# Performance work log

Hardware: AMD Instinct MI355X
Metric: run time of the kernel (lower is better)

Reference implementation:

```python
import jax, jax.numpy as jnp
import numpy as np

DIM = 192; HEADS = 6; WIN = 8; HIDDEN = int(DIM * 2.66); EPS = 1e-5

def dct_matrix(n):
    # DCT-II orthonormal matrix, matches get_dctMatrix(n, n)
    i = np.arange(n)[:, None]; j = np.arange(n)[None, :]
    M = np.cos(np.pi * i * (2 * j + 1) / (2 * n)) * np.sqrt(2.0 / n)
    M[0, :] = np.sqrt(1.0 / n)
    return jnp.asarray(M, dtype=jnp.float32)

def layernorm_c(x, w, b):
    # WithBias LayerNorm over channel dim of BCHW (restormer to_3d/to_4d style)
    mu = x.mean(axis=1, keepdims=True)
    var = ((x - mu) ** 2).mean(axis=1, keepdims=True)
    return (x - mu) / jnp.sqrt(var + EPS) * w[None, :, None, None] + b[None, :, None, None]

def conv1x1(x, w, b=None):
    y = jnp.einsum('oc,bchw->bohw', w, x)
    return y if b is None else y + b[None, :, None, None]

def dwconv3x3(x, w):
    return jax.lax.conv_general_dilated(x, w, (1, 1), ((1, 1), (1, 1)),
        dimension_numbers=('NCHW', 'OIHW', 'NCHW'), feature_group_count=x.shape[1])

def l2norm(x):
    n = jnp.sqrt(jnp.sum(x * x, axis=-1, keepdims=True))
    return x / jnp.maximum(n, 1e-12)

def window_channel_attn(qkv, temperature):
    # 'b (z head c) (h1 h) (w1 w) -> z (b h1 w1) head c (h w)'
    b, _, H, W = qkv.shape
    cph = DIM // HEADS
    h1, w1 = H // WIN, W // WIN
    t = qkv.reshape(b, 3, HEADS, cph, h1, WIN, w1, WIN)
    t = t.transpose(1, 0, 4, 6, 2, 3, 5, 7).reshape(3, b * h1 * w1, HEADS, cph, WIN * WIN)
    q, k, v = t[0], t[1], t[2]
    q = l2norm(q); k = l2norm(k)
    attn = jnp.einsum('nhce,nhde->nhcd', q, k) * temperature[None]  # channel x channel per window
    attn = jax.nn.softmax(attn, axis=-1)
    out = jnp.einsum('nhcd,nhde->nhce', attn, v)
    out = out.reshape(b, h1, w1, HEADS, cph, WIN, WIN)
    out = out.transpose(0, 3, 4, 1, 5, 2, 6).reshape(b, DIM, H, W)
    return out

def forward(x, norm1_w, norm1_b, w_qkv, w_dw, temperature, w_proj, b_proj,
            norm2_w, norm2_b, w_in, w_dwf, w_out):
    B, C, H, W = x.shape
    Mh = dct_matrix(H); Mw = dct_matrix(W)
    # attention branch in DCT domain
    y = layernorm_c(x, norm1_w, norm1_b)
    y = jnp.einsum('ph,bchw->bcpw', Mh, y)      # dct2dx: Mh @ y @ Mw.T
    y = jnp.einsum('bcpw,qw->bcpq', y, Mw)
    qkv = dwconv3x3(conv1x1(y, w_qkv), w_dw)
    a = window_channel_attn(qkv, temperature)
    a = conv1x1(a, w_proj, b_proj)
    a = jnp.einsum('bcpq,qw->bcpw', a, Mw)      # idct2dx: Mh.T @ a @ Mw
    a = jnp.einsum('bcpw,ph->bchw', a, Mh)
    x1 = x + a
    # gated-dconv FFN branch
    z = layernorm_c(x1, norm2_w, norm2_b)
    f = dwconv3x3(conv1x1(z, w_in), w_dwf)
    f1, f2 = jnp.split(f, 2, axis=1)
    f = jax.nn.gelu(f1, approximate=False) * f2
    f = conv1x1(f, w_out)
    return x1 + f

def setup_inputs() -> dict:
    key = jax.random.key(0)
    ks = jax.random.split(key, 8)
    B, C, H, W = 2, DIM, 192, 192
    s = 0.02
    return {
        'x': jax.random.normal(ks[0], (B, C, H, W), jnp.float32),
        'norm1_w': jnp.ones((C,), jnp.float32),
        'norm1_b': jnp.zeros((C,), jnp.float32),
        'w_qkv': jax.random.normal(ks[1], (3 * C, C), jnp.float32) * s,
        'w_dw': jax.random.normal(ks[2], (3 * C, 1, 3, 3), jnp.float32) * s,
        'temperature': jnp.ones((HEADS, 1, 1), jnp.float32) / np.float32(np.sqrt(C)),
        'w_proj': jax.random.normal(ks[3], (C, C), jnp.float32) * s,
        'b_proj': jnp.zeros((C,), jnp.float32),
        'norm2_w': jnp.ones((C,), jnp.float32),
        'norm2_b': jnp.zeros((C,), jnp.float32),
        'w_in': jax.random.normal(ks[4], (2 * HIDDEN, C), jnp.float32) * s,
        'w_dwf': jax.random.normal(ks[5], (2 * HIDDEN, 1, 3, 3), jnp.float32) * s,
        'w_out': jax.random.normal(ks[6], (C, HIDDEN), jnp.float32) * s,
    }

def reference(x, norm1_w, norm1_b, w_qkv, w_dw, temperature, w_proj, b_proj,
              norm2_w, norm2_b, w_in, w_dwf, w_out):
    return forward(x, norm1_w, norm1_b, w_qkv, w_dw, temperature, w_proj, b_proj,
                   norm2_w, norm2_b, w_in, w_dwf, w_out)
```

## Files before the change

### kernel.cpp

```cpp
#include <hip/hip_runtime.h>
#include <hip/hip_bf16.h>

typedef __hip_bfloat16 bft;
typedef __attribute__((ext_vector_type(8))) short bf16x8;
typedef __attribute__((ext_vector_type(4))) float f32x4;

#define BLK 256
static constexpr int Cc = 192;
static constexpr int L  = 192;
static constexpr int S  = 36864;
static constexpr int Bn = 2;
static constexpr int HID = 510;
static constexpr int CH = 64;
static constexpr int FTR = (CH + 2) * L;
static constexpr int GTR = CH * L;
static constexpr double PI_D = 3.141592653589793238462643383279502884;

__device__ __forceinline__ float ldf(const float* p) { return *p; }
__device__ __forceinline__ float ldf(const bft* p)   { return __bfloat162float(*p); }
__device__ __forceinline__ void  stf(float* p, float v) { *p = v; }
__device__ __forceinline__ void  stf(bft* p, float v)   { *p = __float2bfloat16(v); }
__device__ __forceinline__ unsigned short f2bfu(float f) {
    bft h = __float2bfloat16(f);
    return *reinterpret_cast<const unsigned short*>(&h);
}
__device__ __forceinline__ unsigned short bfu(const bft* p) {
    return *reinterpret_cast<const unsigned short*>(p);
}
__device__ __forceinline__ float bu2f(unsigned short u) {
    unsigned int x = (unsigned int)u << 16;
    return __uint_as_float(x);
}
__device__ __forceinline__ bf16x8 ld8(const unsigned short* p) {
    union { unsigned int u[4]; bf16x8 v; } t;
    const unsigned int* q = reinterpret_cast<const unsigned int*>(p);
    t.u[0] = q[0]; t.u[1] = q[1]; t.u[2] = q[2]; t.u[3] = q[3];
    return t.v;
}

__global__ __launch_bounds__(BLK) void k_dct_init(bft* __restrict__ dctb,
                                                  bft* __restrict__ dctTb) {
    int idx = blockIdx.x * BLK + threadIdx.x;
    if (idx >= L * L) return;
    int p = idx / L, h = idx - p * L;
    double v = (p == 0) ? sqrt(1.0 / L)
                        : cos(PI_D * p * (2 * h + 1) / (2.0 * L)) * sqrt(2.0 / L);
    bft bv = __float2bfloat16((float)v);
    dctb[p * L + h] = bv;
    dctTb[h * L + p] = bv;
}

__global__ __launch_bounds__(BLK) void k_cvt(const float* __restrict__ src,
                                             bft* __restrict__ dst,
                                             int Mr, int Kr, int Kp) {
    int idx = blockIdx.x * BLK + threadIdx.x;
    int m = idx / Kp, k = idx - m * Kp;
    float v = (m < Mr && k < Kr) ? src[(size_t)m * Kr + k] : 0.f;
    dst[idx] = __float2bfloat16(v);
}

__global__ __launch_bounds__(BLK) void k_cvt_ffn(const float* __restrict__ src,
                                                 bft* __restrict__ dst) {
    int idx = blockIdx.x * BLK + threadIdx.x;
    int m = idx / Cc, k = idx - m * Cc;
    float v = 0.f;
    if (m < 510) v = src[(size_t)m * Cc + k];
    else if (m >= 512 && m < 1022) v = src[(size_t)(m - 2) * Cc + k];
    dst[idx] = __float2bfloat16(v);
}

template <typename TI>
__global__ __launch_bounds__(BLK) void k_ln8(const TI* __restrict__ x,
                                             const float* __restrict__ w,
                                             const float* __restrict__ b,
                                             bft* __restrict__ out,
                                             long zI, long zO) {
    int t = blockIdx.x * BLK + threadIdx.x;
    int s = t >> 3, u = t & 7;
    const TI* xp = x + (size_t)blockIdx.y * zI + s;
    bft* op = out + (size_t)blockIdx.y * zO;
    float vals[24];
    float sum = 0.f, sq = 0.f;
#pragma unroll
    for (int j = 0; j < 24; ++j) {
        vals[j] = ldf(xp + (size_t)(u * 24 + j) * S);
        sum += vals[j]; sq += vals[j] * vals[j];
    }
#pragma unroll
    for (int m = 1; m < 8; m <<= 1) {
        sum += __shfl_xor(sum, m);
        sq  += __shfl_xor(sq, m);
    }
    float mu = sum * (1.f / Cc);
    float var = sq * (1.f / Cc) - mu * mu;
    float r = rsqrtf(var + 1e-5f);
#pragma unroll
    for (int j = 0; j < 24; ++j) {
        int c = u * 24 + j;
        stf(op + (size_t)c * S + s, (vals[j] - mu) * r * w[c] + b[c]);
    }
}

template <typename TI>
__global__ __launch_bounds__(BLK) void k_lnT8(const TI* __restrict__ x,
                                              const float* __restrict__ w,
                                              const float* __restrict__ b,
                                              bft* __restrict__ out,
                                              long zI, long zO) {
    int t = blockIdx.x * BLK + threadIdx.x;
    int s = t >> 3, u = t & 7;
    const TI* xp = x + (size_t)blockIdx.y * zI + s;
    float vals[24];
    float sum = 0.f, sq = 0.f;
#pragma unroll
    for (int j = 0; j < 24; ++j) {
        vals[j] = ldf(xp + (size_t)(u * 24 + j) * S);
        sum += vals[j]; sq += vals[j] * vals[j];
    }
#pragma unroll
    for (int m = 1; m < 8; m <<= 1) {
        sum += __shfl_xor(sum, m);
        sq  += __shfl_xor(sq, m);
    }
    float mu = sum * (1.f / Cc);
    float var = sq * (1.f / Cc) - mu * mu;
    float r = rsqrtf(var + 1e-5f);
    bft* op = out + (size_t)blockIdx.y * zO + (size_t)s * Cc + u * 24;
#pragma unroll
    for (int q = 0; q < 3; ++q) {
        unsigned short v8[8];
#pragma unroll
        for (int jj = 0; jj < 8; ++jj) {
            int c = u * 24 + q * 8 + jj;
            v8[jj] = f2bfu((vals[q * 8 + jj] - mu) * r * w[c] + b[c]);
        }
        *reinterpret_cast<uint4*>(op + q * 8) = *reinterpret_cast<uint4*>(v8);
    }
}

__global__ __launch_bounds__(BLK) void k_tr(const bft* __restrict__ in,
                                            bft* __restrict__ out, long z) {
    __shared__ unsigned short t[32][72];
    const int tid = threadIdx.x;
    const int s0 = blockIdx.x * 64, c0 = blockIdx.y * 32;
    const bft* ip = in + (size_t)blockIdx.z * z;
    bft* op = out + (size_t)blockIdx.z * z;
    {
        int c = tid >> 3, sc = (tid & 7) * 8;
        *reinterpret_cast<uint4*>(&t[c][sc]) =
            *reinterpret_cast<const uint4*>(ip + (size_t)(c0 + c) * S + s0 + sc);
    }
    __syncthreads();
    {
        int s = tid >> 2, cc = (tid & 3) * 8;
        unsigned short v[8];
#pragma unroll
        for (int q = 0; q < 8; ++q) v[q] = t[cc + q][s];
        *reinterpret_cast<uint4*>(op + (size_t)(s0 + s) * Cc + c0 + cc) =
            *reinterpret_cast<uint4*>(v);
    }
}

template <int WR, int WC, int FM, int FN, int KSTEP, int BMODE, int OMODE,
          bool HASBIAS, bool HASRES, typename OutT, typename ResT>
__global__ __launch_bounds__(256) void k_mm(
    const bft* __restrict__ A, int strideA, int Mreal, long zA,
    const bft* __restrict__ B, int strideB, long zB,
    OutT* __restrict__ Out, int strideO, long zO,
    const float* __restrict__ bias,
    const ResT* __restrict__ Res, long zR,
    int K, int rlo, int rhi) {
    constexpr int BM = WR * FM * 16, BN = WC * FN * 16;
    constexpr int AV = KSTEP / 8;
    __shared__ unsigned short lds[(BM + BN) * (KSTEP + 8)];
    unsigned short (*Al)[KSTEP + 8] =
        reinterpret_cast<unsigned short(*)[KSTEP + 8]>(lds);
    unsigned short (*Bl)[KSTEP + 8] =
        reinterpret_cast<unsigned short(*)[KSTEP + 8]>(lds + BM * (KSTEP + 8));
    const int tid = threadIdx.x;
    const int n0 = blockIdx.x * BN, m0 = blockIdx.y * BM, bz = blockIdx.z;
    const int lane = tid & 63, wv = tid >> 6;
    const int wr = wv / WC, wc = wv % WC;
    const int l15 = lane & 15, l4 = lane >> 4;
    f32x4 acc[FM][FN] = {};

    const bft* Ab = A + (size_t)bz * zA;
    const bft* Bb = B + (size_t)bz * zB;

    for (int k0 = 0; k0 < K; k0 += KSTEP) {
        for (int id = tid; id < BM * AV; id += 256) {
            int row = id / AV, kc = (id % AV) * 8;
            int gm = m0 + row; if (gm >= Mreal) gm = Mreal - 1;
            *reinterpret_cast<uint4*>(&Al[row][kc]) =
                *reinterpret_cast<const uint4*>(Ab + (size_t)gm * strideA + k0 + kc);
        }
        for (int id = tid; id < BN * AV; id += 256) {
            int row = id / AV, kc = (id % AV) * 8;
            int gn = n0 + row;
            uint4 val;
            if constexpr (BMODE == 2) {
                val = *reinterpret_cast<const uint4*>(
                    Bb + (size_t)gn * strideB + k0 + kc);
            } else {
                if (gn >= rlo && gn < rhi)
                    val = *reinterpret_cast<const uint4*>(
                        Bb + (size_t)gn * strideB + k0 + kc);
                else
                    val = make_uint4(0, 0, 0, 0);
            }
            *reinterpret_cast<uint4*>(&Bl[row][kc]) = val;
        }
        __syncthreads();
#pragma unroll
        for (int kk = 0; kk < KSTEP / 32; ++kk) {
            bf16x8 af[FM], bf[FN];
#pragma unroll
            for (int i = 0; i < FM; ++i)
                af[i] = *reinterpret_cast<const bf16x8*>(
                    &Al[wr * FM * 16 + i * 16 + l15][kk * 32 + l4 * 8]);
#pragma unroll
            for (int j = 0; j < FN; ++j)
                bf[j] = *reinterpret_cast<const bf16x8*>(
                    &Bl[wc * FN * 16 + j * 16 + l15][kk * 32 + l4 * 8]);
#pragma unroll
            for (int i = 0; i < FM; ++i)
#pragma unroll
                for (int j = 0; j < FN; ++j)
                    acc[i][j] = __builtin_amdgcn_mfma_f32_16x16x32_bf16(
                        af[i], bf[j], acc[i][j], 0, 0, 0);
        }
        __syncthreads();
    }
    if constexpr (OMODE == 3) {
        constexpr int OST = BM + 8;
        unsigned short* Ol = lds;
#pragma unroll
        for (int i = 0; i < FM; ++i) {
            int mB = wr * FM * 16 + i * 16 + l4 * 4;
#pragma unroll
            for (int j = 0; j < FN; ++j) {
                int n = wc * FN * 16 + j * 16 + l15;
                unsigned short v[4];
#pragma unroll
                for (int r = 0; r < 4; ++r) v[r] = f2bfu(acc[i][j][r]);
                *reinterpret_cast<uint2*>(&Ol[n * OST + mB]) =
                    *reinterpret_cast<uint2*>(v);
            }
        }
        __syncthreads();
        constexpr int TPR = (BM == 128) ? 2 : 1;
        int row = tid / TPR;
        int seg = (TPR == 2) ? (tid & 1) * 64 : 0;
        if (row < BN) {
            bft* dst = (bft*)Out + (size_t)bz * zO
                     + (size_t)(n0 + row) * strideO + m0 + seg;
            const unsigned short* src = &Ol[row * OST + seg];
#pragma unroll
            for (int q = 0; q < 8; ++q)
                *reinterpret_cast<uint4*>(dst + q * 8) =
                    *reinterpret_cast<const uint4*>(src + q * 8);
        }
        return;
    }
#pragma unroll
    for (int i = 0; i < FM; ++i) {
        int mB = m0 + wr * FM * 16 + i * 16 + l4 * 4;
#pragma unroll
        for (int j = 0; j < FN; ++j) {
            int n = n0 + wc * FN * 16 + j * 16 + l15;
#pragma unroll
            for (int r = 0; r < 4; ++r) {
                int m = mB + r;
                if (m >= Mreal) continue;
                float vv = acc[i][j][r];
                if constexpr (HASBIAS) vv += bias[m];
                size_t idx;
                if constexpr (OMODE == 0)
                    idx = (size_t)bz * zO + (size_t)m * strideO + n;
                else {
                    int win = n >> 6, e = n & 63;
                    int hh = ((win / 24) << 3) + (e >> 3);
                    int ww = ((win % 24) << 3) + (e & 7);
                    idx = (size_t)bz * zO + (size_t)m * S + (size_t)hh * L + ww;
                }
                if constexpr (HASRES) vv += ldf(Res + ((OMODE == 0)
                                  ? ((size_t)bz * zR + (size_t)m * strideO + n) : idx));
                stf(Out + idx, vv);
            }
        }
    }
}

__global__ __launch_bounds__(BLK) void k_dwconv(const bft* __restrict__ in,
                                                long inZ,
                                                const float* __restrict__ wt,
                                                bft* __restrict__ out,
                                                long outZ) {
    int t = blockIdx.x * BLK + threadIdx.x;
    int ch2 = t / (S / 8);
    int rem = t - ch2 * (S / 8);
    int b = ch2 / Cc, ch = ch2 - b * Cc;
    int h = rem / 24, wb = (rem - h * 24) * 8;
    const float* wp = wt + (size_t)ch * 9;
    const bft* ip = in + (size_t)b * inZ + (size_t)ch * S;
    float acc[8] = {};
#pragma unroll
    for (int dy = -1; dy <= 1; ++dy) {
        int hh = h + dy;
        if (hh < 0 || hh >= L) continue;
        const bft* rp = ip + hh * L + wb;
        float e[10];
        uint4 mid = *reinterpret_cast<const uint4*>(rp);
        const unsigned short* ms = reinterpret_cast<const unsigned short*>(&mid);
#pragma unroll
        for (int q = 0; q < 8; ++q) e[q + 1] = bu2f(ms[q]);
        e[0] = (wb > 0) ? ldf(rp - 1) : 0.f;
        e[9] = (wb + 8 < L) ? ldf(rp + 8) : 0.f;
        float c0 = wp[(dy + 1) * 3], c1 = wp[(dy + 1) * 3 + 1], c2 = wp[(dy + 1) * 3 + 2];
#pragma unroll
        for (int q = 0; q < 8; ++q)
            acc[q] += c0 * e[q] + c1 * e[q + 1] + c2 * e[q + 2];
    }
    int win = (h >> 3) * 24 + (wb >> 3);
    int e0 = (h & 7) * 8;
    unsigned short ov[8];
#pragma unroll
    for (int q = 0; q < 8; ++q) ov[q] = f2bfu(acc[q]);
    *reinterpret_cast<uint4*>(out + (size_t)b * outZ + (size_t)ch * S + win * 64 + e0) =
        *reinterpret_cast<uint4*>(ov);
}

__global__ __launch_bounds__(256) void k_attn_mfma(
    const bft* __restrict__ QW, long zQ,
    const bft* __restrict__ KW, long zK,
    const bft* __restrict__ VW, long zV,
    const float* __restrict__ temp,
    bft* __restrict__ outp, long zO) {
    __shared__ unsigned short qls[4][32 * 66];
    __shared__ unsigned short kls[4][32 * 66];
    __shared__ unsigned short vls[4][32 * 66];
    __shared__ float rqs[4][32], rks[4][32];
    const int tid = threadIdx.x;
    const int wv = tid >> 6, lane = tid & 63;
    const int win = blockIdx.x * 4 + wv;
    const int hd = blockIdx.y;
    const int bz = blockIdx.z;
    const int l15 = lane & 15, l4 = lane >> 4;
    unsigned short* ql = qls[wv];
    unsigned short* kl = kls[wv];
    unsigned short* vl = vls[wv];
    const size_t base = (size_t)(hd * 32) * S + (size_t)win * 64;

#pragma unroll
    for (int i = 0; i < 4; ++i) {
        int c = i * 8 + (lane >> 3), e0 = (lane & 7) * 8;
        size_t g = base + (size_t)c * S + e0;
        uint4 vq = *reinterpret_cast<const uint4*>(QW + (size_t)bz * zQ + g);
        uint4 vk = *reinterpret_cast<const uint4*>(KW + (size_t)bz * zK + g);
        uint4 vvv = *reinterpret_cast<const uint4*>(VW + (size_t)bz * zV + g);
        unsigned int* dq = reinterpret_cast<unsigned int*>(&ql[c * 66 + e0]);
        unsigned int* dk = reinterpret_cast<unsigned int*>(&kl[c * 66 + e0]);
        unsigned int* dv = reinterpret_cast<unsigned int*>(&vl[c * 66 + e0]);
        dq[0] = vq.x; dq[1] = vq.y; dq[2] = vq.z; dq[3] = vq.w;
        dk[0] = vk.x; dk[1] = vk.y; dk[2] = vk.z; dk[3] = vk.w;
        dv[0] = vvv.x; dv[1] = vvv.y; dv[2] = vvv.z; dv[3] = vvv.w;
    }
    __syncthreads();
    {
        int row = lane & 31;
        const unsigned short* src = (lane < 32) ? ql : kl;
        float s = 0.f;
#pragma unroll
        for (int w = 0; w < 32; ++w) {
            unsigned int d = *reinterpret_cast<const unsigned int*>(&src[row * 66 + 2 * w]);
            float a = bu2f((unsigned short)(d & 0xffff));
            float b = bu2f((unsigned short)(d >> 16));
            s += a * a + b * b;
        }
        float r = 1.f / fmaxf(sqrtf(s), 1e-12f);
        if (lane < 32) rqs[wv][row] = r; else rks[wv][row] = r;
    }
    __syncthreads();
    f32x4 at[2][2] = {};
#pragma unroll
    for (int ks = 0; ks < 2; ++ks) {
        bf16x8 aq[2], bk[2];
#pragma unroll
        for (int i = 0; i < 2; ++i)
            aq[i] = ld8(&ql[(i * 16 + l15) * 66 + ks * 32 + l4 * 8]);
#pragma unroll
        for (int j = 0; j < 2; ++j)
            bk[j] = ld8(&kl[(j * 16 + l15) * 66 + ks * 32 + l4 * 8]);
#pragma unroll
        for (int i = 0; i < 2; ++i)
#pragma unroll
            for (int j = 0; j < 2; ++j)
                at[i][j] = __builtin_amdgcn_mfma_f32_16x16x32_bf16(
                    aq[i], bk[j], at[i][j], 0, 0, 0);
    }
    float tpr = temp[hd];
    float rk0 = rks[wv][l15] * tpr, rk1 = rks[wv][16 + l15] * tpr;
    float pr[2][2][4];
#pragma unroll
    for (int i = 0; i < 2; ++i)
#pragma unroll
        for (int r = 0; r < 4; ++r) {
            int c = i * 16 + l4 * 4 + r;
            float rq = rqs[wv][c];
            float v0 = at[i][0][r] * rq * rk0;
            float v1 = at[i][1][r] * rq * rk1;
            float mx = fmaxf(v0, v1);
#pragma unroll
            for (int m = 1; m < 16; m <<= 1) mx = fmaxf(mx, __shfl_xor(mx, m));
            v0 = __expf(v0 - mx);
            v1 = __expf(v1 - mx);
            float sm = v0 + v1;
#pragma unroll
            for (int m = 1; m < 16; m <<= 1) sm += __shfl_xor(sm, m);
            float inv = 1.f / sm;
            pr[i][0][r] = v0 * inv;
            pr[i][1][r] = v1 * inv;
        }
    __syncthreads();
    unsigned short* pl = ql;
#pragma unroll
    for (int i = 0; i < 2; ++i)
#pragma unroll
        for (int j = 0; j < 2; ++j)
#pragma unroll
            for (int r = 0; r < 4; ++r)
                pl[(i * 16 + l4 * 4 + r) * 34 + j * 16 + l15] = f2bfu(pr[i][j][r]);
    __syncthreads();
    bf16x8 ap[2];
#pragma unroll
    for (int i = 0; i < 2; ++i)
        ap[i] = ld8(&pl[(i * 16 + l15) * 34 + l4 * 8]);
    f32x4 o[2][4] = {};
#pragma unroll
    for (int j = 0; j < 4; ++j) {
        unsigned short tv[8];
#pragma unroll
        for (int q = 0; q < 8; ++q)
            tv[q] = vl[(l4 * 8 + q) * 66 + j * 16 + l15];
        bf16x8 bv = *reinterpret_cast<bf16x8*>(tv);
#pragma unroll
        for (int i = 0; i < 2; ++i)
            o[i][j] = __builtin_amdgcn_mfma_f32_16x16x32_bf16(ap[i], bv, o[i][j], 0, 0, 0);
    }
#pragma unroll
    for (int i = 0; i < 2; ++i)
#pragma unroll
        for (int j = 0; j < 4; ++j) {
            int e = j * 16 + l15, cl = i * 16 + l4 * 4;
            unsigned short v[4];
#pragma unroll
            for (int r = 0; r < 4; ++r) v[r] = f2bfu(o[i][j][r]);
            unsigned short* row = ((e < 32) ? kl : vl) + (e & 31) * 40 + cl;
            *reinterpret_cast<uint2*>(row) = *reinterpret_cast<uint2*>(v);
        }
    {
        const unsigned short* row = ((lane < 32) ? kl : vl) + (lane & 31) * 40;
        bft* dst = outp + (size_t)bz * zO + (size_t)(win * 64 + lane) * Cc + hd * 32;
#pragma unroll
        for (int q = 0; q < 4; ++q)
            *reinterpret_cast<uint4*>(dst + q * 8) =
                *reinterpret_cast<const uint4*>(row + q * 8);
    }
}

__global__ __launch_bounds__(BLK) void k_gateT(const bft* __restrict__ fTg,
                                               const float* __restrict__ wt,
                                               bft* __restrict__ gTg) {
    __shared__ float w1s[64][9];
    __shared__ float w2s[64][9];
    const int tid = threadIdx.x;
    const int cbase = blockIdx.y * 64;
    const bft* fT = fTg + (size_t)blockIdx.z * FTR * 1024;
    bft* gT = gTg + (size_t)blockIdx.z * GTR * 512;
    for (int id = tid; id < 576; id += BLK) {
        int cl = id / 9, k = id - cl * 9;
        int c = cbase + cl;
        w1s[cl][k] = (c < HID) ? wt[(size_t)c * 9 + k] : 0.f;
        w2s[cl][k] = (c < HID) ? wt[(size_t)(c + HID) * 9 + k] : 0.f;
    }
    __syncthreads();
    int px = blockIdx.x * 32 + (tid >> 3);
    int cgl = (tid & 7) * 8;
    int hc = px / L, w = px - hc * L;
    float a1[8] = {}, a2[8] = {};
#pragma unroll
    for (int dy = 0; dy < 3; ++dy) {
#pragma unroll
        for (int dx = 0; dx < 3; ++dx) {
            int ww = w + dx - 1;
            if (ww < 0 || ww >= L) continue;
            size_t frow = (size_t)((hc + dy) * L + ww) * 1024 + cbase + cgl;
            uint4 u1 = *reinterpret_cast<const uint4*>(fT + frow);
            uint4 u2 = *reinterpret_cast<const uint4*>(fT + frow + 512);
            const unsigned short* e1 = reinterpret_cast<const unsigned short*>(&u1);
            const unsigned short* e2 = reinterpret_cast<const unsigned short*>(&u2);
            int k = dy * 3 + dx;
#pragma unroll
            for (int j = 0; j < 8; ++j) {
                a1[j] += w1s[cgl + j][k] * bu2f(e1[j]);
                a2[j] += w2s[cgl + j][k] * bu2f(e2[j]);
            }
        }
    }
    unsigned short ov[8];
#pragma unroll
    for (int j = 0; j < 8; ++j) {
        float ge = 0.5f * a1[j] * (1.f + erff(a1[j] * 0.70710678118654752f));
        ov[j] = f2bfu(ge * a2[j]);
    }
    *reinterpret_cast<uint4*>(gT + (size_t)px * 512 + cbase + cgl) =
        *reinterpret_cast<uint4*>(ov);
}

extern "C" void kernel_launch(void* const* d_in, const int* in_sizes, int n_in,
                              void* d_out, int out_size, void* d_ws, size_t ws_size,
                              hipStream_t stream) {
    const float* x      = (const float*)d_in[0];
    const float* n1w    = (const float*)d_in[1];
    const float* n1b    = (const float*)d_in[2];
    const float* w_qkv  = (const float*)d_in[3];
    const float* w_dw   = (const float*)d_in[4];
    const float* temp   = (const float*)d_in[5];
    const float* w_proj = (const float*)d_in[6];
    const float* b_proj = (const float*)d_in[7];
    const float* n2w    = (const float*)d_in[8];
    const float* n2b    = (const float*)d_in[9];
    const float* w_in   = (const float*)d_in[10];
    const float* w_dwf  = (const float*)d_in[11];
    const float* w_out  = (const float*)d_in[12];
    float* outp = (float*)d_out;

    const long CS = (long)Cc * S;
    const size_t DCT_B = 147456;
    const size_t BUF_B = (size_t)Bn * CS * 2;
    const size_t QKV_B = (size_t)Bn * 3 * CS * 2;
    const size_t WB_B  = 884736;
    const size_t NEED  = DCT_B + 3 * BUF_B + QKV_B + WB_B;
    if (ws_size < NEED) return;

    char* p = (char*)d_ws;
    bft* dctb  = (bft*)p;
    bft* dctTb = dctb + L * L;
    p += DCT_B;
    bft* X1    = (bft*)p;                  p += BUF_B;
    bft* PbB   = (bft*)p;                  p += BUF_B;
    bft* QbB   = (bft*)p;                  p += BUF_B;
    bft* QKV   = (bft*)p;                  p += QKV_B;
    bft* w_qkv_b = (bft*)p;
    bft* w_proj_b = w_qkv_b + 576 * 192;
    bft* w_in_b  = w_proj_b + 192 * 192;
    bft* w_out_b = w_in_b + 1024 * 192;
    bft* fT = QKV;
    bft* gT = QKV + (size_t)Bn * FTR * 1024;
    bft* attnT = QKV + CS;

    k_dct_init<<<144, BLK, 0, stream>>>(dctb, dctTb);
    k_cvt<<<432, BLK, 0, stream>>>(w_qkv, w_qkv_b, 576, 192, 192);
    k_cvt<<<144, BLK, 0, stream>>>(w_proj, w_proj_b, 192, 192, 192);
    k_cvt_ffn<<<768, BLK, 0, stream>>>(w_in, w_in_b);
    k_cvt<<<384, BLK, 0, stream>>>(w_out, w_out_b, 192, 510, 512);

    k_ln8<float><<<dim3(S * 8 / BLK, Bn), BLK, 0, stream>>>(x, n1w, n1b, PbB, CS, CS);
    k_mm<2, 2, 2, 6, 64, 2, 3, false, false, bft, float><<<dim3(1, 3, Bn * Cc), 256, 0, stream>>>(
        PbB, L, L, S,  dctb, L, 0,  QbB, L, S,  nullptr, nullptr, 0,  L, 0, 0);
    k_mm<2, 2, 2, 6, 64, 2, 3, false, false, bft, float><<<dim3(1, 3, Bn * Cc), 256, 0, stream>>>(
        QbB, L, L, S,  dctb, L, 0,  PbB, L, S,  nullptr, nullptr, 0,  L, 0, 0);
    k_tr<<<dim3(576, 6, Bn), BLK, 0, stream>>>(PbB, QbB, CS);
    k_mm<2, 2, 4, 4, 64, 2, 0, false, false, bft, float><<<dim3(288, 5, Bn), 256, 0, stream>>>(
        w_qkv_b, Cc, 576, 0,  QbB, Cc, CS,  QKV, S, 3 * CS,  nullptr, nullptr, 0,  Cc, 0, 0);
    k_dwconv<<<6912, BLK, 0, stream>>>(QKV, 3 * CS, w_dw, PbB, CS);
    k_dwconv<<<6912, BLK, 0, stream>>>(QKV + CS, 3 * CS, w_dw + Cc * 9, QbB, CS);
    k_dwconv<<<6912, BLK, 0, stream>>>(QKV + 2 * CS, 3 * CS, w_dw + 2 * Cc * 9, QKV, 3 * CS);
    k_attn_mfma<<<dim3(144, 6, Bn), 256, 0, stream>>>(
        PbB, CS, QbB, CS, QKV, 3 * CS, temp, attnT, 3 * CS);
    k_mm<2, 2, 4, 4, 64, 2, 2, true, false, bft, float><<<dim3(288, 2, Bn), 256, 0, stream>>>(
        w_proj_b, Cc, Cc, 0,  attnT, Cc, 3 * CS,  QbB, S, CS,  b_proj, nullptr, 0,  Cc, 0, 0);
    k_mm<2, 2, 2, 6, 64, 2, 3, false, false, bft, float><<<dim3(1, 3, Bn * Cc), 256, 0, stream>>>(
        QbB, L, L, S,  dctTb, L, 0,  PbB, L, S,  nullptr, nullptr, 0,  L, 0, 0);
    k_mm<2, 2, 2, 6, 64, 2, 0, false, true, bft, float><<<dim3(1, 3, Bn * Cc), 256, 0, stream>>>(
        dctTb, L, L, 0,  PbB, L, S,  X1, L, S,  nullptr, x, S,  L, 0, 0);

    k_lnT8<bft><<<dim3(S * 8 / BLK, Bn), BLK, 0, stream>>>(X1, n2w, n2b, QbB, CS, CS);
    for (int ck = 0; ck < 3; ++ck) {
        int h0 = ck * CH;
        long off = (long)(h0 - 1) * L;
        int rlo = (h0 == 0) ? L : 0;
        int rhi = (h0 == 2 * CH) ? (FTR - L) : FTR;
        k_mm<2, 2, 4, 4, 64, 4, 3, false, false, bft, float><<<dim3(99, 8, Bn), 256, 0, stream>>>(
            w_in_b, Cc, 1024, 0,  QbB + off * Cc, Cc, CS,  fT, 1024, (long)FTR * 1024,
            nullptr, nullptr, 0,  Cc, rlo, rhi);
        k_gateT<<<dim3(GTR / 32, 8, Bn), BLK, 0, stream>>>(fT, w_dwf, gT);
        k_mm<2, 2, 2, 4, 64, 2, 0, false, true, float, bft><<<dim3(96, 3, Bn), 256, 0, stream>>>(
            w_out_b, 512, 192, 0,  gT, 512, (long)GTR * 512,
            outp + (size_t)h0 * L, S, CS,
            nullptr, X1 + (size_t)h0 * L, CS,  512, 0, 0);
    }
}
```

Before: 768.2 us.

## Add dedicated FFN input projection kernel keeping activation rows resident in LDS

```diff
diff --git a/kernel.cpp b/kernel.cpp
--- a/kernel.cpp
+++ b/kernel.cpp
@@ -291,6 +291,91 @@
     }
 }
 
+__global__ __launch_bounds__(256) void k_ffn_in(
+    const bft* __restrict__ A,
+    const bft* __restrict__ B,
+    long zB,
+    bft* __restrict__ Out, long zO,
+    int rlo, int rhi) {
+    constexpr int BROWS = 64, KF = 192, AST = 72, BST = 200, MT = 128, OST = 136;
+    __shared__ unsigned short Bl[BROWS * BST];
+    __shared__ unsigned short Al[MT * AST];
+    const int tid = threadIdx.x;
+    const int n0 = blockIdx.x * BROWS, bz = blockIdx.z;
+    const int lane = tid & 63, wv = tid >> 6;
+    const int wr = wv >> 1, wc = wv & 1;
+    const int l15 = lane & 15, l4 = lane >> 4;
+    const bft* Bb = B + (size_t)bz * zB;
+    bft* Ob = Out + (size_t)bz * zO;
+
+    for (int id = tid; id < BROWS * (KF / 8); id += 256) {
+        int row = id / 24, kc = (id % 24) * 8;
+        int gn = n0 + row;
+        uint4 val = make_uint4(0, 0, 0, 0);
+        if (gn >= rlo && gn < rhi)
+            val = *reinterpret_cast<const uint4*>(Bb + (size_t)gn * Cc + kc);
+        *reinterpret_cast<uint4*>(&Bl[row * BST + kc]) = val;
+    }
+    __syncthreads();
+
+    for (int mt = 0; mt < 8; ++mt) {
+        f32x4 acc[4][2] = {};
+#pragma unroll
+        for (int ks = 0; ks < 3; ++ks) {
+            for (int id = tid; id < MT * 8; id += 256) {
+                int row = id >> 3, kc = (id & 7) * 8;
+                *reinterpret_cast<uint4*>(&Al[row * AST + kc]) =
+                    *reinterpret_cast<const uint4*>(
+                        A + (size_t)(mt * MT + row) * KF + ks * 64 + kc);
+            }
+            __syncthreads();
+#pragma unroll
+            for (int kk = 0; kk < 2; ++kk) {
+                bf16x8 af[4], bf[2];
+#pragma unroll
+                for (int i = 0; i < 4; ++i)
+                    af[i] = ld8(&Al[(wr * 64 + i * 16 + l15) * AST + kk * 32 + l4 * 8]);
+#pragma unroll
+                for (int j = 0; j < 2; ++j)
+                    bf[j] = ld8(&Bl[(wc * 32 + j * 16 + l15) * BST
+                                    + ks * 64 + kk * 32 + l4 * 8]);
+#pragma unroll
+                for (int i = 0; i < 4; ++i)
+#pragma unroll
+                    for (int j = 0; j < 2; ++j)
+                        acc[i][j] = __builtin_amdgcn_mfma_f32_16x16x32_bf16(
+                            af[i], bf[j], acc[i][j], 0, 0, 0);
+            }
+            __syncthreads();
+        }
+        unsigned short* Ol = Al;
+#pragma unroll
+        for (int i = 0; i < 4; ++i) {
+            int mB = wr * 64 + i * 16 + l4 * 4;
+#pragma unroll
+            for (int j = 0; j < 2; ++j) {
+                int n = wc * 32 + j * 16 + l15;
+                unsigned short v[4];
+#pragma unroll
+                for (int r = 0; r < 4; ++r) v[r] = f2bfu(acc[i][j][r]);
+                *reinterpret_cast<uint2*>(&Ol[n * OST + mB]) =
+                    *reinterpret_cast<uint2*>(v);
+            }
+        }
+        __syncthreads();
+        {
+            int row = tid >> 2, seg = (tid & 3) * 32;
+            bft* dst = Ob + (size_t)(n0 + row) * 1024 + mt * MT + seg;
+            const unsigned short* src = &Ol[row * OST + seg];
+#pragma unroll
+            for (int q = 0; q < 4; ++q)
+                *reinterpret_cast<uint4*>(dst + q * 8) =
+                    *reinterpret_cast<const uint4*>(src + q * 8);
+        }
+        __syncthreads();
+    }
+}
+
 __global__ __launch_bounds__(BLK) void k_dwconv(const bft* __restrict__ in,
                                                 long inZ,
                                                 const float* __restrict__ wt,
@@ -591,9 +676,8 @@
         long off = (long)(h0 - 1) * L;
         int rlo = (h0 == 0) ? L : 0;
         int rhi = (h0 == 2 * CH) ? (FTR - L) : FTR;
-        k_mm<2, 2, 4, 4, 64, 4, 3, false, false, bft, float><<<dim3(99, 8, Bn), 256, 0, stream>>>(
-            w_in_b, Cc, 1024, 0,  QbB + off * Cc, Cc, CS,  fT, 1024, (long)FTR * 1024,
-            nullptr, nullptr, 0,  Cc, rlo, rhi);
+        k_ffn_in<<<dim3(FTR / 64, 1, Bn), 256, 0, stream>>>(
+            w_in_b, QbB + off * Cc, CS, fT, (long)FTR * 1024, rlo, rhi);
         k_gateT<<<dim3(GTR / 32, 8, Bn), BLK, 0, stream>>>(fT, w_dwf, gT);
         k_mm<2, 2, 2, 4, 64, 2, 0, false, true, float, bft><<<dim3(96, 3, Bn), 256, 0, stream>>>(
             w_out_b, 512, 192, 0,  gT, 512, (long)GTR * 512,
```

New measurement: 786.2 us. +2.3%, slower.

## Transpose proj GEMM output layout and keep a bf16 copy of the residual input

Applied to the files above, without the earlier changes.

```diff
diff --git a/kernel.cpp b/kernel.cpp
--- a/kernel.cpp
+++ b/kernel.cpp
@@ -69,21 +69,22 @@
     dst[idx] = __float2bfloat16(v);
 }
 
-template <typename TI>
-__global__ __launch_bounds__(BLK) void k_ln8(const TI* __restrict__ x,
+__global__ __launch_bounds__(BLK) void k_ln8(const float* __restrict__ x,
                                              const float* __restrict__ w,
                                              const float* __restrict__ b,
                                              bft* __restrict__ out,
+                                             bft* __restrict__ xc,
                                              long zI, long zO) {
     int t = blockIdx.x * BLK + threadIdx.x;
     int s = t >> 3, u = t & 7;
-    const TI* xp = x + (size_t)blockIdx.y * zI + s;
+    const float* xp = x + (size_t)blockIdx.y * zI + s;
     bft* op = out + (size_t)blockIdx.y * zO;
+    bft* xp2 = xc + (size_t)blockIdx.y * zO;
     float vals[24];
     float sum = 0.f, sq = 0.f;
 #pragma unroll
     for (int j = 0; j < 24; ++j) {
-        vals[j] = ldf(xp + (size_t)(u * 24 + j) * S);
+        vals[j] = xp[(size_t)(u * 24 + j) * S];
         sum += vals[j]; sq += vals[j] * vals[j];
     }
 #pragma unroll
@@ -98,6 +99,7 @@
     for (int j = 0; j < 24; ++j) {
         int c = u * 24 + j;
         stf(op + (size_t)c * S + s, (vals[j] - mu) * r * w[c] + b[c]);
+        stf(xp2 + (size_t)c * S + s, vals[j]);
     }
 }
 
@@ -161,8 +163,37 @@
     }
 }
 
+__global__ __launch_bounds__(BLK) void k_w2s(const bft* __restrict__ src,
+                                             bft* __restrict__ dst,
+                                             long zI, long zO) {
+    __shared__ unsigned short t[192][100];
+    const int tid = threadIdx.x;
+    const int hh = blockIdx.x;
+    const int ch0 = blockIdx.y * 96;
+    const int bz = blockIdx.z;
+    const int h1 = hh >> 3, ii = hh & 7;
+    const bft* ip = src + (size_t)bz * zI;
+    for (int id = tid; id < 192 * 12; id += BLK) {
+        int r = id / 12, q = id - r * 12;
+        int w1 = r >> 3, jj = r & 7;
+        int s = (h1 * 24 + w1) * 64 + ii * 8 + jj;
+        *reinterpret_cast<uint4*>(&t[r][q * 8]) =
+            *reinterpret_cast<const uint4*>(ip + (size_t)s * Cc + ch0 + q * 8);
+    }
+    __syncthreads();
+    bft* op = dst + (size_t)bz * zO;
+    for (int id = tid; id < 96 * 24; id += BLK) {
+        int c = id / 24, q = id - c * 24;
+        unsigned short v[8];
+#pragma unroll
+        for (int e = 0; e < 8; ++e) v[e] = t[q * 8 + e][c];
+        *reinterpret_cast<uint4*>(op + (size_t)(ch0 + c) * S + (size_t)hh * L + q * 8) =
+            *reinterpret_cast<uint4*>(v);
+    }
+}
+
 template <int WR, int WC, int FM, int FN, int KSTEP, int BMODE, int OMODE,
-          bool HASBIAS, bool HASRES, typename OutT, typename ResT>
+          bool HASBIAS, bool BIASN, bool HASRES, typename OutT, typename ResT>
 __global__ __launch_bounds__(256) void k_mm(
     const bft* __restrict__ A, int strideA, int Mreal, long zA,
     const bft* __restrict__ B, int strideB, long zB,
@@ -273,7 +304,7 @@
                 int m = mB + r;
                 if (m >= Mreal) continue;
                 float vv = acc[i][j][r];
-                if constexpr (HASBIAS) vv += bias[m];
+                if constexpr (HASBIAS) vv += BIASN ? bias[n] : bias[m];
                 size_t idx;
                 if constexpr (OMODE == 0)
                     idx = (size_t)bz * zO + (size_t)m * strideO + n;
@@ -540,7 +571,7 @@
     const size_t BUF_B = (size_t)Bn * CS * 2;
     const size_t QKV_B = (size_t)Bn * 3 * CS * 2;
     const size_t WB_B  = 884736;
-    const size_t NEED  = DCT_B + 3 * BUF_B + QKV_B + WB_B;
+    const size_t NEED  = DCT_B + 4 * BUF_B + QKV_B + WB_B;
     if (ws_size < NEED) return;
 
     char* p = (char*)d_ws;
@@ -550,6 +581,7 @@
     bft* X1    = (bft*)p;                  p += BUF_B;
     bft* PbB   = (bft*)p;                  p += BUF_B;
     bft* QbB   = (bft*)p;                  p += BUF_B;
+    bft* XC    = (bft*)p;                  p += BUF_B;
     bft* QKV   = (bft*)p;                  p += QKV_B;
     bft* w_qkv_b = (bft*)p;
     bft* w_proj_b = w_qkv_b + 576 * 192;
@@ -565,25 +597,26 @@
     k_cvt_ffn<<<768, BLK, 0, stream>>>(w_in, w_in_b);
     k_cvt<<<384, BLK, 0, stream>>>(w_out, w_out_b, 192, 510, 512);
 
-    k_ln8<float><<<dim3(S * 8 / BLK, Bn), BLK, 0, stream>>>(x, n1w, n1b, PbB, CS, CS);
-    k_mm<2, 2, 2, 6, 64, 2, 3, false, false, bft, float><<<dim3(1, 3, Bn * Cc), 256, 0, stream>>>(
+    k_ln8<<<dim3(S * 8 / BLK, Bn), BLK, 0, stream>>>(x, n1w, n1b, PbB, XC, CS, CS);
+    k_mm<2, 2, 2, 6, 64, 2, 3, false, false, false, bft, float><<<dim3(1, 3, Bn * Cc), 256, 0, stream>>>(
         PbB, L, L, S,  dctb, L, 0,  QbB, L, S,  nullptr, nullptr, 0,  L, 0, 0);
-    k_mm<2, 2, 2, 6, 64, 2, 3, false, false, bft, float><<<dim3(1, 3, Bn * Cc), 256, 0, stream>>>(
+    k_mm<2, 2, 2, 6, 64, 2, 3, false, false, false, bft, float><<<dim3(1, 3, Bn * Cc), 256, 0, stream>>>(
         QbB, L, L, S,  dctb, L, 0,  PbB, L, S,  nullptr, nullptr, 0,  L, 0, 0);
     k_tr<<<dim3(576, 6, Bn), BLK, 0, stream>>>(PbB, QbB, CS);
-    k_mm<2, 2, 4, 4, 64, 2, 0, false, false, bft, float><<<dim3(288, 5, Bn), 256, 0, stream>>>(
+    k_mm<2, 2, 4, 4, 64, 2, 0, false, false, false, bft, float><<<dim3(288, 5, Bn), 256, 0, stream>>>(
         w_qkv_b, Cc, 576, 0,  QbB, Cc, CS,  QKV, S, 3 * CS,  nullptr, nullptr, 0,  Cc, 0, 0);
     k_dwconv<<<6912, BLK, 0, stream>>>(QKV, 3 * CS, w_dw, PbB, CS);
     k_dwconv<<<6912, BLK, 0, stream>>>(QKV + CS, 3 * CS, w_dw + Cc * 9, QbB, CS);
     k_dwconv<<<6912, BLK, 0, stream>>>(QKV + 2 * CS, 3 * CS, w_dw + 2 * Cc * 9, QKV, 3 * CS);
     k_attn_mfma<<<dim3(144, 6, Bn), 256, 0, stream>>>(
         PbB, CS, QbB, CS, QKV, 3 * CS, temp, attnT, 3 * CS);
-    k_mm<2, 2, 4, 4, 64, 2, 2, true, false, bft, float><<<dim3(288, 2, Bn), 256, 0, stream>>>(
-        w_proj_b, Cc, Cc, 0,  attnT, Cc, 3 * CS,  QbB, S, CS,  b_proj, nullptr, 0,  Cc, 0, 0);
-    k_mm<2, 2, 2, 6, 64, 2, 3, false, false, bft, float><<<dim3(1, 3, Bn * Cc), 256, 0, stream>>>(
+    k_mm<2, 2, 2, 6, 64, 2, 0, true, true, false, bft, float><<<dim3(1, 576, Bn), 256, 0, stream>>>(
+        attnT, Cc, S, 3 * CS,  w_proj_b, Cc, 0,  PbB, Cc, CS,  b_proj, (const float*)nullptr, 0,  Cc, 0, 0);
+    k_w2s<<<dim3(192, 2, Bn), BLK, 0, stream>>>(PbB, QbB, CS, CS);
+    k_mm<2, 2, 2, 6, 64, 2, 3, false, false, false, bft, float><<<dim3(1, 3, Bn * Cc), 256, 0, stream>>>(
         QbB, L, L, S,  dctTb, L, 0,  PbB, L, S,  nullptr, nullptr, 0,  L, 0, 0);
-    k_mm<2, 2, 2, 6, 64, 2, 0, false, true, bft, float><<<dim3(1, 3, Bn * Cc), 256, 0, stream>>>(
-        dctTb, L, L, 0,  PbB, L, S,  X1, L, S,  nullptr, x, S,  L, 0, 0);
+    k_mm<2, 2, 2, 6, 64, 2, 0, false, false, true, bft, bft><<<dim3(1, 3, Bn * Cc), 256, 0, stream>>>(
+        dctTb, L, L, 0,  PbB, L, S,  X1, L, S,  nullptr, XC, S,  L, 0, 0);
 
     k_lnT8<bft><<<dim3(S * 8 / BLK, Bn), BLK, 0, stream>>>(X1, n2w, n2b, QbB, CS, CS);
     for (int ck = 0; ck < 3; ++ck) {
@@ -591,11 +624,11 @@
         long off = (long)(h0 - 1) * L;
         int rlo = (h0 == 0) ? L : 0;
         int rhi = (h0 == 2 * CH) ? (FTR - L) : FTR;
-        k_mm<2, 2, 4, 4, 64, 4, 3, false, false, bft, float><<<dim3(99, 8, Bn), 256, 0, stream>>>(
+        k_mm<2, 2, 4, 4, 64, 4, 3, false, false, false, bft, float><<<dim3(99, 8, Bn), 256, 0, stream>>>(
             w_in_b, Cc, 1024, 0,  QbB + off * Cc, Cc, CS,  fT, 1024, (long)FTR * 1024,
             nullptr, nullptr, 0,  Cc, rlo, rhi);
         k_gateT<<<dim3(GTR / 32, 8, Bn), BLK, 0, stream>>>(fT, w_dwf, gT);
-        k_mm<2, 2, 2, 4, 64, 2, 0, false, true, float, bft><<<dim3(96, 3, Bn), 256, 0, stream>>>(
+        k_mm<2, 2, 2, 4, 64, 2, 0, false, false, true, float, bft><<<dim3(96, 3, Bn), 256, 0, stream>>>(
             w_out_b, 512, 192, 0,  gT, 512, (long)GTR * 512,
             outp + (size_t)h0 * L, S, CS,
             nullptr, X1 + (size_t)h0 * L, CS,  512, 0, 0);
```

After: 796.0 us. 3.6% more time.
